# Kernel tuning notes

Measured on AMD Instinct MI355X. Metric: run time of the kernel, lower is better.

## Reference

```python
import jax, jax.numpy as jnp
import numpy as np

K = 3  # polynomial filter order

def gfgcn_layer(X, S, W, h, b):
    # X: [N, in], W: [in, out], h: [K], b: [out]
    X = X @ W
    X_out = h[0] * X
    Sx = X
    for k in range(1, K):
        Sx = S @ Sx                 # graph shift propagation
        X_out = X_out + h[k] * Sx   # scalar-weighted accumulate
    return X_out + b[None, :]


def setup_inputs() -> dict:
    key = jax.random.key(0)
    ks = jax.random.split(key, 12)
    N, in_dim, hid_dim, out_dim = 8192, 512, 128, 64
    # scale S so repeated propagation stays numerically tame
    S = jax.random.normal(ks[0], (N, N), dtype=jnp.float32) / jnp.sqrt(jnp.float32(N))
    X = jax.random.normal(ks[1], (N, in_dim), dtype=jnp.float32)
    def kaiming(k, shape):
        bound = np.sqrt(6.0 / shape[0])
        return jax.random.uniform(k, shape, jnp.float32, -bound, bound)
    W1 = kaiming(ks[2], (in_dim, hid_dim))
    W2 = kaiming(ks[3], (hid_dim, hid_dim))
    W3 = kaiming(ks[4], (hid_dim, out_dim))
    h1 = jnp.ones((K,), jnp.float32)
    h2 = jnp.ones((K,), jnp.float32)
    h3 = jnp.ones((K,), jnp.float32)
    b1 = jnp.zeros((hid_dim,), jnp.float32)
    b2 = jnp.zeros((hid_dim,), jnp.float32)
    b3 = jnp.zeros((out_dim,), jnp.float32)
    return {"S": S, "X": X, "W1": W1, "h1": h1, "b1": b1,
            "W2": W2, "h2": h2, "b2": b2, "W3": W3, "h3": h3, "b3": b3}


def reference(S, X, W1, h1, b1, W2, h2, b2, W3, h3, b3):
    # layer 1 + ReLU (dropout p=0 -> identity, batch_norm=False)
    X = jax.nn.relu(gfgcn_layer(X, S, W1, h1, b1))
    # layer 2 + ReLU
    X = jax.nn.relu(gfgcn_layer(X, S, W2, h2, b2))
    # last layer, last_act = Identity
    return gfgcn_layer(X, S, W3, h3, b3)
```

## Files before the change

### kernel.cpp

```cpp
#include <hip/hip_runtime.h>


typedef __attribute__((ext_vector_type(4))) float  f32x4;
typedef __attribute__((ext_vector_type(8))) __bf16 bf16x8;
typedef __attribute__((ext_vector_type(4))) __bf16 bf16x4;

__device__ __forceinline__ void gload_lds16(const __bf16* g, __bf16* l) {
    __builtin_amdgcn_global_load_lds(
        (const __attribute__((address_space(1))) void*)g,
        (__attribute__((address_space(3))) void*)l, 16, 0, 0);
}

__global__ void cvt_f32_bf16(const float4* __restrict__ in,
                             bf16x4* __restrict__ out, int n4) {
    int i  = blockIdx.x * blockDim.x + threadIdx.x;
    int st = gridDim.x * blockDim.x;
    for (; i < n4; i += st) {
        float4 v = in[i];
        bf16x4 o;
        o[0] = (__bf16)v.x; o[1] = (__bf16)v.y;
        o[2] = (__bf16)v.z; o[3] = (__bf16)v.w;
        out[i] = o;
    }
}

__global__ void cvt_transpose(const float* __restrict__ W,
                              __bf16* __restrict__ Wt, int Kd, int Md) {
    int i = blockIdx.x * blockDim.x + threadIdx.x;
    if (i < Kd * Md) {
        int k = i / Md, m = i % Md;
        Wt[(size_t)m * Kd + k] = (__bf16)W[i];
    }
}

template<int MF, int NF, int OUTMODE>
__global__ __launch_bounds__(256)
void gemm_rd(const __bf16* __restrict__ A, const __bf16* __restrict__ Bt,
             void* __restrict__ out, int K, int Kchunk, int Mtot, int Ntot)
{
    const int lane = threadIdx.x & 63;
    const int w    = threadIdx.x >> 6;
    const int l15  = lane & 15;
    const int quad = lane >> 4;

    const int m_base = blockIdx.x * (64 * MF) + w * (16 * MF);
    const int n_base = blockIdx.y * (16 * NF);
    const int kstart = blockIdx.z * Kchunk;

    const __bf16* Ap[MF];
    #pragma unroll
    for (int mf = 0; mf < MF; mf++)
        Ap[mf] = A + (size_t)(m_base + mf * 16 + l15) * K + kstart + quad * 8;
    const __bf16* Bp[NF];
    #pragma unroll
    for (int nf = 0; nf < NF; nf++)
        Bp[nf] = Bt + (size_t)(n_base + nf * 16 + l15) * K + kstart + quad * 8;

    f32x4 acc[MF][NF];
    #pragma unroll
    for (int mf = 0; mf < MF; mf++)
        #pragma unroll
        for (int nf = 0; nf < NF; nf++)
            acc[mf][nf] = (f32x4){0.f, 0.f, 0.f, 0.f};

    #pragma unroll 2
    for (int ks = 0; ks < Kchunk; ks += 32) {
        bf16x8 a[MF], b[NF];
        #pragma unroll
        for (int mf = 0; mf < MF; mf++) a[mf] = *(const bf16x8*)(Ap[mf] + ks);
        #pragma unroll
        for (int nf = 0; nf < NF; nf++) b[nf] = *(const bf16x8*)(Bp[nf] + ks);
        #pragma unroll
        for (int mf = 0; mf < MF; mf++)
            #pragma unroll
            for (int nf = 0; nf < NF; nf++)
                acc[mf][nf] = __builtin_amdgcn_mfma_f32_16x16x32_bf16(
                    a[mf], b[nf], acc[mf][nf], 0, 0, 0);
    }

    if (OUTMODE == 0) {
        float* P = (float*)out + (size_t)blockIdx.z * Mtot * Ntot;
        #pragma unroll
        for (int mf = 0; mf < MF; mf++) {
            const int rowb = m_base + mf * 16 + quad * 4;
            #pragma unroll
            for (int nf = 0; nf < NF; nf++) {
                const int col = n_base + nf * 16 + l15;
                *(f32x4*)(P + (size_t)col * Mtot + rowb) = acc[mf][nf];
            }
        }
    } else {
        __bf16* O = (__bf16*)out;
        #pragma unroll
        for (int mf = 0; mf < MF; mf++) {
            const int rowb = m_base + mf * 16 + quad * 4;
            #pragma unroll
            for (int nf = 0; nf < NF; nf++) {
                const int col = n_base + nf * 16 + l15;
                #pragma unroll
                for (int r = 0; r < 4; r++)
                    O[(size_t)(rowb + r) * Ntot + col] = (__bf16)acc[mf][nf][r];
            }
        }
    }
}

template<int NFW>
__global__ __launch_bounds__(256)
void sgemm_lds(const __bf16* __restrict__ A, const __bf16* __restrict__ Bt,
               float* __restrict__ P, int K, int Kchunk, int Mtot)
{
    constexpr int BN = 32 * NFW;
    __shared__ __bf16 Asm[2][64 * 32];
    __shared__ __bf16 Bsm[2][BN * 32];

    const int t    = threadIdx.x;
    const int lane = t & 63;
    const int w    = t >> 6;
    const int wm   = w >> 1;
    const int wn   = w & 1;
    const int l15  = lane & 15;
    const int quad = lane >> 4;

    const int m_block = blockIdx.x * 64;
    const int kstart  = blockIdx.z * Kchunk;

    const int rt  = t >> 2;
    const int qs  = (t & 3) ^ ((rt >> 1) & 3);
    const __bf16* gA  = A  + (size_t)(m_block + rt) * K + kstart + qs * 8;
    const __bf16* gB0 = Bt + (size_t)rt * K        + kstart + qs * 8;
    const __bf16* gB1 = Bt + (size_t)(64 + rt) * K + kstart + qs * 8;

    f32x4 acc[2][NFW];
    #pragma unroll
    for (int mf = 0; mf < 2; mf++)
        #pragma unroll
        for (int nf = 0; nf < NFW; nf++)
            acc[mf][nf] = (f32x4){0.f, 0.f, 0.f, 0.f};

    auto stage = [&](int buf, int ks) {
        gload_lds16(gA  + ks, &Asm[buf][t * 8]);
        gload_lds16(gB0 + ks, &Bsm[buf][t * 8]);
        if (NFW == 4)
            gload_lds16(gB1 + ks, &Bsm[buf][2048 + t * 8]);
    };

    int aoff[2], boff[NFW];
    #pragma unroll
    for (int mf = 0; mf < 2; mf++) {
        const int ar = wm * 32 + mf * 16 + l15;
        aoff[mf] = ar * 32 + (quad ^ ((ar >> 1) & 3)) * 8;
    }
    #pragma unroll
    for (int nf = 0; nf < NFW; nf++) {
        const int br = wn * 16 * NFW + nf * 16 + l15;
        boff[nf] = br * 32 + (quad ^ ((br >> 1) & 3)) * 8;
    }

    stage(0, 0);
    __syncthreads();

    int buf = 0;
    for (int ks = 0; ; ) {
        const int nks = ks + 32;
        if (nks < Kchunk) stage(buf ^ 1, nks);

        bf16x8 a[2], b[NFW];
        #pragma unroll
        for (int mf = 0; mf < 2; mf++)
            a[mf] = *(const bf16x8*)&Asm[buf][aoff[mf]];
        #pragma unroll
        for (int nf = 0; nf < NFW; nf++)
            b[nf] = *(const bf16x8*)&Bsm[buf][boff[nf]];

        #pragma unroll
        for (int mf = 0; mf < 2; mf++)
            #pragma unroll
            for (int nf = 0; nf < NFW; nf++)
                acc[mf][nf] = __builtin_amdgcn_mfma_f32_16x16x32_bf16(
                    a[mf], b[nf], acc[mf][nf], 0, 0, 0);

        ks = nks;
        if (ks >= Kchunk) break;
        __syncthreads();
        buf ^= 1;
    }

    float* Pz = P + (size_t)blockIdx.z * Mtot * BN;
    #pragma unroll
    for (int mf = 0; mf < 2; mf++) {
        const int rowb = m_block + wm * 32 + mf * 16 + quad * 4;
        #pragma unroll
        for (int nf = 0; nf < NFW; nf++) {
            const int col = wn * 16 * NFW + nf * 16 + l15;
            *(f32x4*)(Pz + (size_t)col * Mtot + rowb) = acc[mf][nf];
        }
    }
}

__global__ void reduce_partials(const float* __restrict__ P,
                                __bf16* __restrict__ Y, int total4,
                                int SP, int MN) {
    int i = blockIdx.x * blockDim.x + threadIdx.x;
    if (i >= total4) return;
    size_t base = (size_t)i * 4;
    float4 s = *(const float4*)(P + base);
    for (int sp = 1; sp < SP; sp++) {
        float4 v = *(const float4*)(P + (size_t)sp * MN + base);
        s.x += v.x; s.y += v.y; s.z += v.z; s.w += v.w;
    }
    bf16x4 o; o[0] = (__bf16)s.x; o[1] = (__bf16)s.y;
    o[2] = (__bf16)s.z; o[3] = (__bf16)s.w;
    *(bf16x4*)(Y + base) = o;
}

template<int RELU, int F32OUT>
__global__ void combine_out(const float* __restrict__ P,
                            const __bf16* __restrict__ Y0t,
                            const __bf16* __restrict__ Y1t,
                            const float* __restrict__ h,
                            const float* __restrict__ bias,
                            void* __restrict__ outp,
                            int F, int SP) {
    const int i = blockIdx.x * blockDim.x + threadIdx.x;
    const int total = F * 2048;
    if (i >= total) return;
    const int f  = i >> 11;
    const int n4 = i & 2047;
    const size_t base = (size_t)f * 8192 + (size_t)n4 * 4;
    const int MN = F * 8192;

    float4 s = *(const float4*)(P + base);
    for (int sp = 1; sp < SP; sp++) {
        float4 v = *(const float4*)(P + (size_t)sp * MN + base);
        s.x += v.x; s.y += v.y; s.z += v.z; s.w += v.w;
    }
    bf16x4 y0 = *(const bf16x4*)(Y0t + base);
    bf16x4 y1 = *(const bf16x4*)(Y1t + base);
    const float h0 = h[0], h1 = h[1], h2 = h[2], bb = bias[f];

    float v[4] = {s.x, s.y, s.z, s.w};
    #pragma unroll
    for (int r = 0; r < 4; r++) {
        float x = h0 * (float)y0[r] + h1 * (float)y1[r] + h2 * v[r] + bb;
        if (RELU) x = fmaxf(x, 0.0f);
        v[r] = x;
    }
    const int node = n4 * 4;
    if (F32OUT) {
        float* O = (float*)outp;
        #pragma unroll
        for (int r = 0; r < 4; r++) O[(size_t)(node + r) * F + f] = v[r];
    } else {
        __bf16* O = (__bf16*)outp;
        #pragma unroll
        for (int r = 0; r < 4; r++) O[(size_t)(node + r) * F + f] = (__bf16)v[r];
    }
}

extern "C" void kernel_launch(void* const* d_in, const int* in_sizes, int n_in,
                              void* d_out, int out_size, void* d_ws, size_t ws_size,
                              hipStream_t stream) {
    const float* S  = (const float*)d_in[0];
    const float* X  = (const float*)d_in[1];
    const float* W1 = (const float*)d_in[2];
    const float* h1 = (const float*)d_in[3];
    const float* b1 = (const float*)d_in[4];
    const float* W2 = (const float*)d_in[5];
    const float* h2 = (const float*)d_in[6];
    const float* b2 = (const float*)d_in[7];
    const float* W3 = (const float*)d_in[8];
    const float* h3 = (const float*)d_in[9];
    const float* b3 = (const float*)d_in[10];
    float* out = (float*)d_out;

    const int Nn = 8192, IN = 512, HID = 128, OUT = 64;

    char* ws = (char*)d_ws;
    size_t off = 0;
    auto carve = [&](size_t bytes) -> void* {
        void* p = ws + off;
        off += (bytes + 255) & ~(size_t)255;
        return p;
    };
    __bf16* Sb  = (__bf16*)carve((size_t)Nn * Nn  * 2);
    __bf16* Xb  = (__bf16*)carve((size_t)Nn * IN  * 2);
    __bf16* W1t = (__bf16*)carve((size_t)IN  * HID * 2);
    __bf16* W2t = (__bf16*)carve((size_t)HID * HID * 2);
    __bf16* W3t = (__bf16*)carve((size_t)HID * OUT * 2);
    __bf16* Y0t = (__bf16*)carve((size_t)HID * Nn * 2);
    __bf16* Y1t = (__bf16*)carve((size_t)HID * Nn * 2);
    __bf16* Act = (__bf16*)carve((size_t)Nn * HID * 2);
    size_t  base = off;

    const size_t per_split = (size_t)HID * Nn * 4;
    int SP = 1;
    while (SP < 8 && base + (size_t)(SP * 2) * per_split <= ws_size) SP *= 2;
    float* P = (float*)carve((size_t)SP * per_split);
    const int KCH = Nn / SP;

    {
        int n4 = Nn * Nn / 4;
        cvt_f32_bf16<<<dim3((n4 + 255) / 256), dim3(256), 0, stream>>>(
            (const float4*)S, (bf16x4*)Sb, n4);
        n4 = Nn * IN / 4;
        cvt_f32_bf16<<<dim3((n4 + 255) / 256), dim3(256), 0, stream>>>(
            (const float4*)X, (bf16x4*)Xb, n4);
    }
    cvt_transpose<<<dim3((IN * HID + 255) / 256), dim3(256), 0, stream>>>(W1, W1t, IN, HID);
    cvt_transpose<<<dim3((HID * HID + 255) / 256), dim3(256), 0, stream>>>(W2, W2t, HID, HID);
    cvt_transpose<<<dim3((HID * OUT + 255) / 256), dim3(256), 0, stream>>>(W3, W3t, HID, OUT);

    auto sgemm = [&](const __bf16* Bt, int F) {
        if (F == 128)
            sgemm_lds<4><<<dim3(Nn / 64, 1, SP), dim3(256), 0, stream>>>(
                Sb, Bt, P, Nn, KCH, Nn);
        else
            sgemm_lds<2><<<dim3(Nn / 64, 1, SP), dim3(256), 0, stream>>>(
                Sb, Bt, P, Nn, KCH, Nn);
    };
    auto reduceY = [&](__bf16* Y, int F) {
        int t4 = F * 2048;
        reduce_partials<<<dim3((t4 + 255) / 256), dim3(256), 0, stream>>>(
            P, Y, t4, SP, F * Nn);
    };

    gemm_rd<2, 4, 1><<<dim3(1, Nn / 64, 1), dim3(256), 0, stream>>>(
        W1t, Xb, Y0t, IN, IN, HID, Nn);
    sgemm(Y0t, HID);
    reduceY(Y1t, HID);
    sgemm(Y1t, HID);
    combine_out<1, 0><<<dim3(HID * 2048 / 256), dim3(256), 0, stream>>>(
        P, Y0t, Y1t, h1, b1, Act, HID, SP);

    gemm_rd<2, 4, 1><<<dim3(1, Nn / 64, 1), dim3(256), 0, stream>>>(
        W2t, Act, Y0t, HID, HID, HID, Nn);
    sgemm(Y0t, HID);
    reduceY(Y1t, HID);
    sgemm(Y1t, HID);
    combine_out<1, 0><<<dim3(HID * 2048 / 256), dim3(256), 0, stream>>>(
        P, Y0t, Y1t, h2, b2, Act, HID, SP);

    gemm_rd<1, 4, 1><<<dim3(1, Nn / 64, 1), dim3(256), 0, stream>>>(
        W3t, Act, Y0t, HID, HID, OUT, Nn);
    sgemm(Y0t, OUT);
    reduceY(Y1t, OUT);
    sgemm(Y1t, OUT);
    combine_out<0, 1><<<dim3(OUT * 2048 / 256), dim3(256), 0, stream>>>(
        P, Y0t, Y1t, h3, b3, out, OUT, SP);

    (void)in_sizes; (void)n_in; (void)out_size;
}
```

Measured before the change: 710.4 us.

## Fuse fp32-to-bf16 conversion of S and X into first GEMMs

Removes the standalone conversion kernels for S and X. The first S-propagation GEMM now reads fp32 S directly, converts it to bf16 in registers, stages it into LDS and also writes the bf16 copy out for the later GEMMs. The first X@W1 GEMM reads fp32 X and converts it on the fly. This saves one full read and write pass over the 256 MB fp32 S and two kernel launches. In exchange, the first S GEMM does synchronous loads, where the other S GEMMs use async global-to-LDS loads.

```diff
diff --git a/kernel.cpp b/kernel.cpp
--- a/kernel.cpp
+++ b/kernel.cpp
@@ -9,19 +9,6 @@
     __builtin_amdgcn_global_load_lds(
         (const __attribute__((address_space(1))) void*)g,
         (__attribute__((address_space(3))) void*)l, 16, 0, 0);
-}
-
-__global__ void cvt_f32_bf16(const float4* __restrict__ in,
-                             bf16x4* __restrict__ out, int n4) {
-    int i  = blockIdx.x * blockDim.x + threadIdx.x;
-    int st = gridDim.x * blockDim.x;
-    for (; i < n4; i += st) {
-        float4 v = in[i];
-        bf16x4 o;
-        o[0] = (__bf16)v.x; o[1] = (__bf16)v.y;
-        o[2] = (__bf16)v.z; o[3] = (__bf16)v.w;
-        out[i] = o;
-    }
 }
 
 __global__ void cvt_transpose(const float* __restrict__ W,
@@ -33,9 +20,9 @@
     }
 }
 
-template<int MF, int NF, int OUTMODE>
+template<int MF, int NF, int OUTMODE, int BF32>
 __global__ __launch_bounds__(256)
-void gemm_rd(const __bf16* __restrict__ A, const __bf16* __restrict__ Bt,
+void gemm_rd(const __bf16* __restrict__ A, const void* __restrict__ Bv,
              void* __restrict__ out, int K, int Kchunk, int Mtot, int Ntot)
 {
     const int lane = threadIdx.x & 63;
@@ -51,10 +38,15 @@
     #pragma unroll
     for (int mf = 0; mf < MF; mf++)
         Ap[mf] = A + (size_t)(m_base + mf * 16 + l15) * K + kstart + quad * 8;
+
     const __bf16* Bp[NF];
-    #pragma unroll
-    for (int nf = 0; nf < NF; nf++)
-        Bp[nf] = Bt + (size_t)(n_base + nf * 16 + l15) * K + kstart + quad * 8;
+    const float*  Bpf[NF];
+    #pragma unroll
+    for (int nf = 0; nf < NF; nf++) {
+        const size_t roff = (size_t)(n_base + nf * 16 + l15) * K + kstart + quad * 8;
+        if (BF32) Bpf[nf] = (const float*)Bv + roff;
+        else      Bp[nf]  = (const __bf16*)Bv + roff;
+    }
 
     f32x4 acc[MF][NF];
     #pragma unroll
@@ -69,7 +61,20 @@
         #pragma unroll
         for (int mf = 0; mf < MF; mf++) a[mf] = *(const bf16x8*)(Ap[mf] + ks);
         #pragma unroll
-        for (int nf = 0; nf < NF; nf++) b[nf] = *(const bf16x8*)(Bp[nf] + ks);
+        for (int nf = 0; nf < NF; nf++) {
+            if (BF32) {
+                float4 f0 = *(const float4*)(Bpf[nf] + ks);
+                float4 f1 = *(const float4*)(Bpf[nf] + ks + 4);
+                bf16x8 t;
+                t[0] = (__bf16)f0.x; t[1] = (__bf16)f0.y;
+                t[2] = (__bf16)f0.z; t[3] = (__bf16)f0.w;
+                t[4] = (__bf16)f1.x; t[5] = (__bf16)f1.y;
+                t[6] = (__bf16)f1.z; t[7] = (__bf16)f1.w;
+                b[nf] = t;
+            } else {
+                b[nf] = *(const bf16x8*)(Bp[nf] + ks);
+            }
+        }
         #pragma unroll
         for (int mf = 0; mf < MF; mf++)
             #pragma unroll
@@ -105,10 +110,11 @@
     }
 }
 
-template<int NFW>
+template<int NFW, int CVT>
 __global__ __launch_bounds__(256)
-void sgemm_lds(const __bf16* __restrict__ A, const __bf16* __restrict__ Bt,
-               float* __restrict__ P, int K, int Kchunk, int Mtot)
+void sgemm_lds(const void* __restrict__ Av, const __bf16* __restrict__ Bt,
+               float* __restrict__ P, __bf16* __restrict__ Sb_out,
+               int K, int Kchunk, int Mtot)
 {
     constexpr int BN = 32 * NFW;
     __shared__ __bf16 Asm[2][64 * 32];
@@ -127,7 +133,11 @@
 
     const int rt  = t >> 2;
     const int qs  = (t & 3) ^ ((rt >> 1) & 3);
-    const __bf16* gA  = A  + (size_t)(m_block + rt) * K + kstart + qs * 8;
+
+    const __bf16* gA  = (const __bf16*)Av + (size_t)(m_block + rt) * K + kstart + qs * 8;
+    const float*  gAf = (const float*)Av  + (size_t)(m_block + rt) * K + kstart + qs * 8;
+    __bf16* sbo = CVT ? (Sb_out + (size_t)(m_block + rt) * K + kstart + qs * 8) : nullptr;
+
     const __bf16* gB0 = Bt + (size_t)rt * K        + kstart + qs * 8;
     const __bf16* gB1 = Bt + (size_t)(64 + rt) * K + kstart + qs * 8;
 
@@ -139,7 +149,19 @@
             acc[mf][nf] = (f32x4){0.f, 0.f, 0.f, 0.f};
 
     auto stage = [&](int buf, int ks) {
-        gload_lds16(gA  + ks, &Asm[buf][t * 8]);
+        if (CVT) {
+            float4 f0 = *(const float4*)(gAf + ks);
+            float4 f1 = *(const float4*)(gAf + ks + 4);
+            bf16x8 c;
+            c[0] = (__bf16)f0.x; c[1] = (__bf16)f0.y;
+            c[2] = (__bf16)f0.z; c[3] = (__bf16)f0.w;
+            c[4] = (__bf16)f1.x; c[5] = (__bf16)f1.y;
+            c[6] = (__bf16)f1.z; c[7] = (__bf16)f1.w;
+            *(bf16x8*)&Asm[buf][t * 8] = c;
+            *(bf16x8*)(sbo + ks) = c;
+        } else {
+            gload_lds16(gA + ks, &Asm[buf][t * 8]);
+        }
         gload_lds16(gB0 + ks, &Bsm[buf][t * 8]);
         if (NFW == 4)
             gload_lds16(gB1 + ks, &Bsm[buf][2048 + t * 8]);
@@ -284,7 +306,6 @@
         return p;
     };
     __bf16* Sb  = (__bf16*)carve((size_t)Nn * Nn  * 2);
-    __bf16* Xb  = (__bf16*)carve((size_t)Nn * IN  * 2);
     __bf16* W1t = (__bf16*)carve((size_t)IN  * HID * 2);
     __bf16* W2t = (__bf16*)carve((size_t)HID * HID * 2);
     __bf16* W3t = (__bf16*)carve((size_t)HID * OUT * 2);
@@ -299,25 +320,17 @@
     float* P = (float*)carve((size_t)SP * per_split);
     const int KCH = Nn / SP;
 
-    {
-        int n4 = Nn * Nn / 4;
-        cvt_f32_bf16<<<dim3((n4 + 255) / 256), dim3(256), 0, stream>>>(
-            (const float4*)S, (bf16x4*)Sb, n4);
-        n4 = Nn * IN / 4;
-        cvt_f32_bf16<<<dim3((n4 + 255) / 256), dim3(256), 0, stream>>>(
-            (const float4*)X, (bf16x4*)Xb, n4);
-    }
     cvt_transpose<<<dim3((IN * HID + 255) / 256), dim3(256), 0, stream>>>(W1, W1t, IN, HID);
     cvt_transpose<<<dim3((HID * HID + 255) / 256), dim3(256), 0, stream>>>(W2, W2t, HID, HID);
     cvt_transpose<<<dim3((HID * OUT + 255) / 256), dim3(256), 0, stream>>>(W3, W3t, HID, OUT);
 
     auto sgemm = [&](const __bf16* Bt, int F) {
         if (F == 128)
-            sgemm_lds<4><<<dim3(Nn / 64, 1, SP), dim3(256), 0, stream>>>(
-                Sb, Bt, P, Nn, KCH, Nn);
+            sgemm_lds<4, 0><<<dim3(Nn / 64, 1, SP), dim3(256), 0, stream>>>(
+                Sb, Bt, P, nullptr, Nn, KCH, Nn);
         else
-            sgemm_lds<2><<<dim3(Nn / 64, 1, SP), dim3(256), 0, stream>>>(
-                Sb, Bt, P, Nn, KCH, Nn);
+            sgemm_lds<2, 0><<<dim3(Nn / 64, 1, SP), dim3(256), 0, stream>>>(
+                Sb, Bt, P, nullptr, Nn, KCH, Nn);
     };
     auto reduceY = [&](__bf16* Y, int F) {
         int t4 = F * 2048;
@@ -325,15 +338,16 @@
             P, Y, t4, SP, F * Nn);
     };
 
-    gemm_rd<2, 4, 1><<<dim3(1, Nn / 64, 1), dim3(256), 0, stream>>>(
-        W1t, Xb, Y0t, IN, IN, HID, Nn);
-    sgemm(Y0t, HID);
+    gemm_rd<2, 4, 1, 1><<<dim3(1, Nn / 64, 1), dim3(256), 0, stream>>>(
+        W1t, X, Y0t, IN, IN, HID, Nn);
+    sgemm_lds<4, 1><<<dim3(Nn / 64, 1, SP), dim3(256), 0, stream>>>(
+        S, Y0t, P, Sb, Nn, KCH, Nn);
     reduceY(Y1t, HID);
     sgemm(Y1t, HID);
     combine_out<1, 0><<<dim3(HID * 2048 / 256), dim3(256), 0, stream>>>(
         P, Y0t, Y1t, h1, b1, Act, HID, SP);
 
-    gemm_rd<2, 4, 1><<<dim3(1, Nn / 64, 1), dim3(256), 0, stream>>>(
+    gemm_rd<2, 4, 1, 0><<<dim3(1, Nn / 64, 1), dim3(256), 0, stream>>>(
         W2t, Act, Y0t, HID, HID, HID, Nn);
     sgemm(Y0t, HID);
     reduceY(Y1t, HID);
@@ -341,7 +355,7 @@
     combine_out<1, 0><<<dim3(HID * 2048 / 256), dim3(256), 0, stream>>>(
         P, Y0t, Y1t, h2, b2, Act, HID, SP);
 
-    gemm_rd<1, 4, 1><<<dim3(1, Nn / 64, 1), dim3(256), 0, stream>>>(
+    gemm_rd<1, 4, 1, 0><<<dim3(1, Nn / 64, 1), dim3(256), 0, stream>>>(
         W3t, Act, Y0t, HID, HID, OUT, Nn);
     sgemm(Y0t, OUT);
     reduceY(Y1t, OUT);
```

New measurement: 737.1 us. +3.8%, slower.
